# Kernel optimization log

Hardware: AMD Instinct MI355X
Metric: run time of the kernel (lower is better)

The kernel has to match this reference:

```python
import jax, jax.numpy as jnp
import numpy as np

N = 40000      # nodes
E = 640000     # edges
G = 2048       # graphs
D = 128        # emb_dim
T = 10         # num_tasks
L = 5          # layers
ATOM_VOCAB = 64
BOND_VOCAB = 8
BN_EPS = 1e-5


def _bn(x, g, b, m, v):
    # inference-mode BatchNorm1d with running stats
    return (x - m) * jax.lax.rsqrt(v + BN_EPS) * g + b


def setup_inputs() -> dict:
    key = jax.random.key(0)
    ks = jax.random.split(key, 24)
    inp = {
        "x_atom": jax.random.randint(ks[0], (N, 9), 0, ATOM_VOCAB),
        "edge_index": jax.random.randint(ks[1], (2, E), 0, N),
        "edge_attr": jax.random.randint(ks[2], (E, 3), 0, BOND_VOCAB),
        "batch": jnp.sort(jax.random.randint(ks[3], (N,), 0, G)),
        # embedding tables
        "atom_emb": jax.random.normal(ks[4], (9, ATOM_VOCAB, D)) * 0.1,
        "bond_emb": jax.random.normal(ks[5], (L, 3, BOND_VOCAB, D)) * 0.1,
        # per-layer GIN params (stacked over L)
        "eps": jnp.zeros((L,)),
        "W1": jax.random.normal(ks[6], (L, D, 2 * D)) * 0.05,
        "b1": jnp.zeros((L, 2 * D)),
        "g1": jnp.ones((L, 2 * D)),
        "bt1": jnp.zeros((L, 2 * D)),
        "m1": jax.random.normal(ks[7], (L, 2 * D)) * 0.1,
        "v1": jax.random.uniform(ks[8], (L, 2 * D), minval=0.5, maxval=1.5),
        "W2": jax.random.normal(ks[9], (L, 2 * D, D)) * 0.05,
        "b2": jnp.zeros((L, D)),
        # outer BatchNorm per layer
        "gO": jnp.ones((L, D)),
        "btO": jnp.zeros((L, D)),
        "mO": jax.random.normal(ks[10], (L, D)) * 0.1,
        "vO": jax.random.uniform(ks[11], (L, D), minval=0.5, maxval=1.5),
        # prediction head
        "Wp": jax.random.normal(ks[12], (D, T)) * 0.05,
        "bp": jnp.zeros((T,)),
    }
    return inp


def reference(x_atom, edge_index, edge_attr, batch, atom_emb, bond_emb, eps,
              W1, b1, g1, bt1, m1, v1, W2, b2, gO, btO, mO, vO, Wp, bp):
    src, dst = edge_index[0], edge_index[1]
    # AtomEncoder: sum of per-feature embeddings -> [N, D]
    x = atom_emb[jnp.arange(9)[None, :], x_atom].sum(axis=1)
    feat3 = jnp.arange(3)[None, :]
    for i in range(L):
        # BondEncoder for this layer -> [E, D]
        e = bond_emb[i][feat3, edge_attr].sum(axis=1)
        # message: relu(x_j + edge_emb); aggregate: scatter-add at dst
        msg = jax.nn.relu(x[src] + e)
        agg = jax.ops.segment_sum(msg, dst, num_segments=N)
        h = (1.0 + eps[i]) * x + agg
        # MLP: Linear -> BN -> ReLU -> Linear
        h = jax.nn.relu(_bn(h @ W1[i] + b1[i], g1[i], bt1[i], m1[i], v1[i]))
        h = h @ W2[i] + b2[i]
        # outer BN; ReLU after all but last layer (dropout = identity in eval)
        x = _bn(h, gO[i], btO[i], mO[i], vO[i])
        if i < L - 1:
            x = jax.nn.relu(x)
    # global mean pool over graphs
    sums = jax.ops.segment_sum(x, batch, num_segments=G)
    cnt = jax.ops.segment_sum(jnp.ones((N,), x.dtype), batch, num_segments=G)
    pooled = sums / jnp.maximum(cnt, 1.0)[:, None]
    return pooled @ Wp + bp
```

## Files before the change

kernel.cpp:

```cpp
#include <hip/hip_runtime.h>
#include <hip/hip_bf16.h>

#define NN 40000
#define NE 640000
#define NG 2048
#define DD 128
#define NT 10
#define NL 5
#define NB 80

typedef __attribute__((ext_vector_type(8))) short short8;
typedef __attribute__((ext_vector_type(4))) float f32x4;
typedef unsigned short ushort_t;

static __device__ __forceinline__ ushort_t f2b(float f) {
    return __bfloat16_as_ushort(__float2bfloat16(f));
}
static __device__ __forceinline__ float b2f(ushort_t u) {
    return __bfloat162float(__ushort_as_bfloat16(u));
}

__global__ void k_atom(const int* __restrict__ xa, const float* __restrict__ emb,
                       ushort_t* __restrict__ x16) {
    int n = blockIdx.x, d = threadIdx.x;
    __shared__ int idx[9];
    if (d < 9) idx[d] = xa[n * 9 + d];
    __syncthreads();
    float s = 0.f;
#pragma unroll
    for (int f = 0; f < 9; ++f) s += emb[(f * 64 + idx[f]) * DD + d];
    x16[n * DD + d] = f2b(s);
}


__global__ void k_hist(const int* __restrict__ ei, int* __restrict__ deg) {
    int e = blockIdx.x * 256 + threadIdx.x;
    atomicAdd(&deg[ei[NE + e]], 1);
}

__global__ void k_scan1(const int* __restrict__ deg, int* __restrict__ off,
                        int* __restrict__ blksum) {
    int b = blockIdx.x, t = threadIdx.x;
    int i = b * 256 + t;
    __shared__ int s[256];
    int v = (i < NN) ? deg[i] : 0;
    s[t] = v;
    __syncthreads();
    for (int d = 1; d < 256; d <<= 1) {
        int add = (t >= d) ? s[t - d] : 0;
        __syncthreads();
        s[t] += add;
        __syncthreads();
    }
    if (i <= NN) off[i] = s[t] - v;
    if (t == 255) blksum[b] = s[255];
}

__global__ void k_scan2(int* __restrict__ blk) {
    int t = threadIdx.x;
    __shared__ int s[256];
    int v = blk[t];
    s[t] = v;
    __syncthreads();
    for (int d = 1; d < 256; d <<= 1) {
        int add = (t >= d) ? s[t - d] : 0;
        __syncthreads();
        s[t] += add;
        __syncthreads();
    }
    blk[256 + t] = s[t] - v;
}

__global__ void k_scan3(int* __restrict__ off, const int* __restrict__ blk) {
    int b = blockIdx.x, t = threadIdx.x;
    int i = b * 256 + t;
    if (i <= NN) off[i] += blk[256 + b];
}

__global__ void __launch_bounds__(256)
k_bucket(const int* __restrict__ ei, const int* __restrict__ ea,
         const int* __restrict__ off, int* __restrict__ gbk,
         int2* __restrict__ ebuf) {
    __shared__ int hist[NB];
    __shared__ int sbase[NB];
    int t = threadIdx.x;
    int e0 = blockIdx.x * 1024;
    if (t < NB) hist[t] = 0;
    __syncthreads();
    int rank[4], buck[4], rec[4], dstv[4];
#pragma unroll
    for (int k = 0; k < 4; ++k) {
        int e = e0 + k * 256 + t;
        int src = ei[e];
        int dst = ei[NE + e];
        int a0 = ea[e * 3 + 0], a1 = ea[e * 3 + 1], a2 = ea[e * 3 + 2];
        rec[k] = src | ((a0 | (a1 << 3) | (a2 << 6)) << 16);
        dstv[k] = dst;
        int b = dst >> 9;
        buck[k] = b;
        rank[k] = atomicAdd(&hist[b], 1);
    }
    __syncthreads();
    if (t < NB) sbase[t] = atomicAdd(&gbk[t], hist[t]);
    __syncthreads();
#pragma unroll
    for (int k = 0; k < 4; ++k) {
        int b = buck[k];
        int slot = off[b << 9] + sbase[b] + rank[k];
        ebuf[slot] = make_int2(rec[k], dstv[k]);
    }
}

__global__ void k_scatter2(const int2* __restrict__ ebuf, const int* __restrict__ off,
                           int* __restrict__ cursor, int2* __restrict__ epack) {
    int i = blockIdx.x * 256 + threadIdx.x;
    int2 s = ebuf[i];
    int dst = s.y;
    int p = off[dst] + atomicAdd(&cursor[dst], 1);
    epack[p] = make_int2(s.x & 0xFFFF, s.x >> 16);
}

__global__ void k_tables(const float* __restrict__ W1, const float* __restrict__ W2,
                         const float* __restrict__ bemb, ushort_t* __restrict__ W1P,
                         ushort_t* __restrict__ W2P, ushort_t* __restrict__ ebsum16) {
    int tid = blockIdx.x * 256 + threadIdx.x;
    int layer = tid >> 16;
    int r = tid & 65535;
    int half = r >> 15;
    int q = r & 32767;
    int j = q & 7;
    int lane = (q >> 3) & 63;
    if (half == 0) {
        int kk = (q >> 9) & 3;
        int nt = q >> 11;
        int n = nt * 16 + (lane & 15);
        int k = kk * 32 + (lane >> 4) * 8 + j;
        W1P[layer * 32768 + q] = f2b(W1[(layer * DD + k) * 256 + n]);
    } else {
        int kk = (q >> 9) & 7;
        int nt = q >> 12;
        int n = nt * 16 + (lane & 15);
        int k = kk * 32 + (lane >> 4) * 8 + j;
        W2P[layer * 32768 + q] = f2b(W2[(layer * 256 + k) * DD + n]);
    }
    int d = tid & 127;
    int c = (tid >> 7) & 511;
    const float* bl = bemb + (size_t)layer * 3 * 8 * DD;
    ebsum16[tid] = f2b(bl[(c & 7) * DD + d] + bl[(8 + ((c >> 3) & 7)) * DD + d] +
                       bl[(16 + (c >> 6)) * DD + d]);
}

__global__ void __launch_bounds__(256)
k_gather(const ushort_t* __restrict__ xin, const int* __restrict__ off,
         const int2* __restrict__ epack, const ushort_t* __restrict__ ebsum16,
         const float* __restrict__ eps, int layer, ushort_t* __restrict__ h16) {
    int t = threadIdx.x;
    int lane = t & 63;
    int n = blockIdx.x * 4 + (t >> 6);
    const ushort2* x2 = (const ushort2*)xin;
    const ushort2* eb2 = (const ushort2*)ebsum16;
    ushort2 xv = x2[n * 64 + lane];
    float es = 1.f + eps[layer];
    float ax = es * b2f(xv.x), ay = es * b2f(xv.y);
    int p = off[n], p1 = off[n + 1];

    int2 e0, e1, e2, e3;
    bool have = (p + 4 <= p1);
    if (have) { e0 = epack[p]; e1 = epack[p + 1]; e2 = epack[p + 2]; e3 = epack[p + 3]; }
    while (have) {
        int np = p + 4;
        bool nh = (np + 4 <= p1);
        int2 f0, f1, f2, f3;
        if (nh) { f0 = epack[np]; f1 = epack[np + 1]; f2 = epack[np + 2]; f3 = epack[np + 3]; }
        ushort2 v0 = eb2[e0.y * 64 + lane];
        ushort2 s0 = x2[e0.x * 64 + lane];
        ushort2 v1 = eb2[e1.y * 64 + lane];
        ushort2 s1 = x2[e1.x * 64 + lane];
        ushort2 v2 = eb2[e2.y * 64 + lane];
        ushort2 s2 = x2[e2.x * 64 + lane];
        ushort2 v3 = eb2[e3.y * 64 + lane];
        ushort2 s3 = x2[e3.x * 64 + lane];
        ax += fmaxf(b2f(v0.x) + b2f(s0.x), 0.f) + fmaxf(b2f(v1.x) + b2f(s1.x), 0.f) +
              fmaxf(b2f(v2.x) + b2f(s2.x), 0.f) + fmaxf(b2f(v3.x) + b2f(s3.x), 0.f);
        ay += fmaxf(b2f(v0.y) + b2f(s0.y), 0.f) + fmaxf(b2f(v1.y) + b2f(s1.y), 0.f) +
              fmaxf(b2f(v2.y) + b2f(s2.y), 0.f) + fmaxf(b2f(v3.y) + b2f(s3.y), 0.f);
        p = np;
        e0 = f0; e1 = f1; e2 = f2; e3 = f3;
        have = nh;
    }
    for (; p < p1; ++p) {
        int2 er = epack[p];
        ushort2 ev = eb2[er.y * 64 + lane];
        ushort2 sv = x2[er.x * 64 + lane];
        ax += fmaxf(b2f(ev.x) + b2f(sv.x), 0.f);
        ay += fmaxf(b2f(ev.y) + b2f(sv.y), 0.f);
    }
    ushort2 o;
    o.x = f2b(ax);
    o.y = f2b(ay);
    ((ushort2*)h16)[n * 64 + lane] = o;
}

__global__ void __launch_bounds__(256)
k_mlp_mfma(const ushort_t* __restrict__ h16, const ushort_t* __restrict__ W1P,
           const ushort_t* __restrict__ W2P, const float* __restrict__ b1,
           const float* __restrict__ g1, const float* __restrict__ bt1,
           const float* __restrict__ m1, const float* __restrict__ v1,
           const float* __restrict__ b2_, const float* __restrict__ gO,
           const float* __restrict__ btO, const float* __restrict__ mO,
           const float* __restrict__ vO, int relu, ushort_t* __restrict__ xout) {
    __shared__ ushort_t aS[32 * 136];
    __shared__ ushort_t mid[32 * 264];
    int t = threadIdx.x;
    int wave = t >> 6, lane = t & 63;
    int row0 = blockIdx.x * 32;
    int lrow = lane & 15, quad = lane >> 4;

#pragma unroll
    for (int ps = 0; ps < 2; ++ps) {
        int idx = ps * 256 + t;
        int r = idx >> 4, c = (idx & 15) * 8;
        *(short8*)&aS[r * 136 + c] = *(const short8*)&h16[(row0 + r) * DD + c];
    }
    __syncthreads();

    f32x4 acc1[2][4];
#pragma unroll
    for (int rt = 0; rt < 2; ++rt)
#pragma unroll
        for (int i = 0; i < 4; ++i) acc1[rt][i] = (f32x4){0.f, 0.f, 0.f, 0.f};
#pragma unroll
    for (int kk = 0; kk < 4; ++kk) {
        short8 af0 = *(const short8*)&aS[lrow * 136 + kk * 32 + quad * 8];
        short8 af1 = *(const short8*)&aS[(16 + lrow) * 136 + kk * 32 + quad * 8];
#pragma unroll
        for (int i = 0; i < 4; ++i) {
            int nt = wave * 4 + i;
            short8 bf = *(const short8*)&W1P[((nt * 4 + kk) * 64 + lane) * 8];
            acc1[0][i] = __builtin_amdgcn_mfma_f32_16x16x32_bf16(af0, bf, acc1[0][i], 0, 0, 0);
            acc1[1][i] = __builtin_amdgcn_mfma_f32_16x16x32_bf16(af1, bf, acc1[1][i], 0, 0, 0);
        }
    }
#pragma unroll
    for (int i = 0; i < 4; ++i) {
        int col = (wave * 4 + i) * 16 + lrow;
        float s1 = g1[col] * rsqrtf(v1[col] + 1e-5f);
        float sh = bt1[col] - (m1[col] - b1[col]) * s1;
#pragma unroll
        for (int rt = 0; rt < 2; ++rt)
#pragma unroll
            for (int r = 0; r < 4; ++r) {
                int row = rt * 16 + quad * 4 + r;
                float o = acc1[rt][i][r] * s1 + sh;
                mid[row * 264 + col] = f2b(fmaxf(o, 0.f));
            }
    }
    __syncthreads();

    f32x4 acc2[2][2];
#pragma unroll
    for (int rt = 0; rt < 2; ++rt)
#pragma unroll
        for (int i = 0; i < 2; ++i) acc2[rt][i] = (f32x4){0.f, 0.f, 0.f, 0.f};
#pragma unroll
    for (int kk = 0; kk < 8; ++kk) {
        short8 af0 = *(const short8*)&mid[lrow * 264 + kk * 32 + quad * 8];
        short8 af1 = *(const short8*)&mid[(16 + lrow) * 264 + kk * 32 + quad * 8];
#pragma unroll
        for (int i = 0; i < 2; ++i) {
            int nt = wave * 2 + i;
            short8 bf = *(const short8*)&W2P[((nt * 8 + kk) * 64 + lane) * 8];
            acc2[0][i] = __builtin_amdgcn_mfma_f32_16x16x32_bf16(af0, bf, acc2[0][i], 0, 0, 0);
            acc2[1][i] = __builtin_amdgcn_mfma_f32_16x16x32_bf16(af1, bf, acc2[1][i], 0, 0, 0);
        }
    }
#pragma unroll
    for (int i = 0; i < 2; ++i) {
        int col = (wave * 2 + i) * 16 + lrow;
        float s = gO[col] * rsqrtf(vO[col] + 1e-5f);
        float sh = btO[col] - (mO[col] - b2_[col]) * s;
#pragma unroll
        for (int rt = 0; rt < 2; ++rt)
#pragma unroll
            for (int r = 0; r < 4; ++r) {
                int row = rt * 16 + quad * 4 + r;
                float o = acc2[rt][i][r] * s + sh;
                if (relu) o = fmaxf(o, 0.f);
                xout[(row0 + row) * DD + col] = f2b(o);
            }
    }
}

__global__ void k_pool(const ushort_t* __restrict__ x16, const int* __restrict__ batch,
                       float* __restrict__ pooled) {
    int g = blockIdx.x, d = threadIdx.x;
    int lo = 0, hi = NN;
    while (lo < hi) { int m = (lo + hi) >> 1; if (batch[m] < g) lo = m + 1; else hi = m; }
    int start = lo;
    hi = NN;
    while (lo < hi) { int m = (lo + hi) >> 1; if (batch[m] < g + 1) lo = m + 1; else hi = m; }
    int end = lo;
    float s = 0.f;
    for (int n = start; n < end; ++n) s += b2f(x16[n * DD + d]);
    float c = fmaxf((float)(end - start), 1.f);
    pooled[g * DD + d] = s / c;
}

__global__ void k_head(const float* __restrict__ pooled, const float* __restrict__ Wp,
                       const float* __restrict__ bp, float* __restrict__ out) {
    int g = blockIdx.x;
    int d = threadIdx.x;
    __shared__ float p[DD];
    p[d] = pooled[g * DD + d];
    __syncthreads();
    if (d < NT) {
        float acc = bp[d];
#pragma unroll 8
        for (int k = 0; k < DD; ++k) acc = fmaf(p[k], Wp[k * NT + d], acc);
        out[g * NT + d] = acc;
    }
}

extern "C" void kernel_launch(void* const* d_in, const int* in_sizes, int n_in,
                              void* d_out, int out_size, void* d_ws, size_t ws_size,
                              hipStream_t stream) {
    const int* x_atom = (const int*)d_in[0];
    const int* edge_index = (const int*)d_in[1];
    const int* edge_attr = (const int*)d_in[2];
    const int* batch = (const int*)d_in[3];
    const float* atom_emb = (const float*)d_in[4];
    const float* bond_emb = (const float*)d_in[5];
    const float* eps = (const float*)d_in[6];
    const float* W1 = (const float*)d_in[7];
    const float* b1 = (const float*)d_in[8];
    const float* g1 = (const float*)d_in[9];
    const float* bt1 = (const float*)d_in[10];
    const float* m1 = (const float*)d_in[11];
    const float* v1 = (const float*)d_in[12];
    const float* W2 = (const float*)d_in[13];
    const float* b2 = (const float*)d_in[14];
    const float* gO = (const float*)d_in[15];
    const float* btO = (const float*)d_in[16];
    const float* mO = (const float*)d_in[17];
    const float* vO = (const float*)d_in[18];
    const float* Wp = (const float*)d_in[19];
    const float* bp = (const float*)d_in[20];

    ushort_t* x16a = (ushort_t*)d_ws;
    ushort_t* x16b = x16a + NN * DD;
    ushort_t* h16 = x16b + NN * DD;
    float* pooled = (float*)(h16 + NN * DD);
    ushort_t* W1P = (ushort_t*)(pooled + NG * DD);
    ushort_t* W2P = W1P + NL * 32768;
    ushort_t* ebsum16 = W2P + NL * 32768;
    int* deg = (int*)(ebsum16 + NL * 65536);
    int* off = deg + NN;
    int* blk = off + 40064;
    int* cursor = blk + 512;
    int* gbk = cursor + NN;
    int2* epack = (int2*)(gbk + 128);
    int2* ebuf = epack + NE;

    hipMemsetAsync(deg, 0, (NN + 40064 + 512 + NN + 128) * sizeof(int), stream);

    k_tables<<<NL * 65536 / 256, 256, 0, stream>>>(W1, W2, bond_emb, W1P, W2P, ebsum16);
    k_atom<<<NN, DD, 0, stream>>>(x_atom, atom_emb, x16a);

    k_hist<<<NE / 256, 256, 0, stream>>>(edge_index, deg);
    k_scan1<<<157, 256, 0, stream>>>(deg, off, blk);
    k_scan2<<<1, 256, 0, stream>>>(blk);
    k_scan3<<<157, 256, 0, stream>>>(off, blk);
    k_bucket<<<NE / 1024, 256, 0, stream>>>(edge_index, edge_attr, off, gbk, ebuf);
    k_scatter2<<<NE / 256, 256, 0, stream>>>(ebuf, off, cursor, epack);

    for (int i = 0; i < NL; ++i) {
        ushort_t* xin = (i & 1) ? x16b : x16a;
        ushort_t* xout = (i & 1) ? x16a : x16b;
        k_gather<<<NN / 4, 256, 0, stream>>>(xin, off, epack, ebsum16 + i * 65536,
                                             eps, i, h16);
        k_mlp_mfma<<<NN / 32, 256, 0, stream>>>(
            h16, W1P + (size_t)i * 32768, W2P + (size_t)i * 32768, b1 + i * 256,
            g1 + i * 256, bt1 + i * 256, m1 + i * 256, v1 + i * 256, b2 + i * DD,
            gO + i * DD, btO + i * DD, mO + i * DD, vO + i * DD,
            (i < NL - 1) ? 1 : 0, xout);
    }
    k_pool<<<NG, DD, 0, stream>>>(x16b, batch, pooled);
    k_head<<<NG, DD, 0, stream>>>(pooled, Wp, bp, (float*)d_out);
}
```

Before: 435.7 us.

## Fuse setup kernels, merge pool+head, and deepen gather edge prefetch to 8

Merges the table-prep, atom-embedding and degree-histogram kernels into one launch with block-range dispatch, and fuses mean pooling with the prediction head so the pooled buffer is no longer written and reread. The gather loop now prefetches edge records 8 at a time with clamped indices and a predicated tail, replacing the 4-wide loop plus scalar remainder. This raises memory-level parallelism in the main gather and cuts launch overhead. The cost is redundant loads for short adjacency lists and more register pressure in the gather.

```diff
diff --git a/kernel.cpp b/kernel.cpp
--- a/kernel.cpp
+++ b/kernel.cpp
@@ -20,23 +20,56 @@
     return __bfloat162float(__ushort_as_bfloat16(u));
 }
 
-__global__ void k_atom(const int* __restrict__ xa, const float* __restrict__ emb,
-                       ushort_t* __restrict__ x16) {
-    int n = blockIdx.x, d = threadIdx.x;
-    __shared__ int idx[9];
-    if (d < 9) idx[d] = xa[n * 9 + d];
-    __syncthreads();
-    float s = 0.f;
-#pragma unroll
-    for (int f = 0; f < 9; ++f) s += emb[(f * 64 + idx[f]) * DD + d];
-    x16[n * DD + d] = f2b(s);
-}
-
-
-__global__ void k_hist(const int* __restrict__ ei, int* __restrict__ deg) {
-    int e = blockIdx.x * 256 + threadIdx.x;
-    atomicAdd(&deg[ei[NE + e]], 1);
-}
+__global__ void __launch_bounds__(256)
+k_setup(const float* __restrict__ W1, const float* __restrict__ W2,
+        const float* __restrict__ bemb, const int* __restrict__ xa,
+        const float* __restrict__ aemb, const int* __restrict__ ei,
+        ushort_t* __restrict__ W1P, ushort_t* __restrict__ W2P,
+        ushort_t* __restrict__ ebsum16, ushort_t* __restrict__ x16,
+        int* __restrict__ deg) {
+    int b = blockIdx.x, t = threadIdx.x;
+    if (b < 1280) {
+        int tid = b * 256 + t;
+        int layer = tid >> 16;
+        int r = tid & 65535;
+        int half = r >> 15;
+        int q = r & 32767;
+        int j = q & 7;
+        int lane = (q >> 3) & 63;
+        if (half == 0) {
+            int kk = (q >> 9) & 3;
+            int nt = q >> 11;
+            int n = nt * 16 + (lane & 15);
+            int k = kk * 32 + (lane >> 4) * 8 + j;
+            W1P[layer * 32768 + q] = f2b(W1[(layer * DD + k) * 256 + n]);
+        } else {
+            int kk = (q >> 9) & 7;
+            int nt = q >> 12;
+            int n = nt * 16 + (lane & 15);
+            int k = kk * 32 + (lane >> 4) * 8 + j;
+            W2P[layer * 32768 + q] = f2b(W2[(layer * 256 + k) * DD + n]);
+        }
+        int d = tid & 127;
+        int c = (tid >> 7) & 511;
+        const float* bl = bemb + (size_t)layer * 3 * 8 * DD;
+        ebsum16[tid] = f2b(bl[(c & 7) * DD + d] + bl[(8 + ((c >> 3) & 7)) * DD + d] +
+                           bl[(16 + (c >> 6)) * DD + d]);
+    } else if (b < 21280) {
+        int half = t >> 7, d = t & 127;
+        int n = (b - 1280) * 2 + half;
+        __shared__ int idx[2][9];
+        if (d < 9) idx[half][d] = xa[n * 9 + d];
+        __syncthreads();
+        float s = 0.f;
+#pragma unroll
+        for (int f = 0; f < 9; ++f) s += aemb[(f * 64 + idx[half][f]) * DD + d];
+        x16[n * DD + d] = f2b(s);
+    } else {
+        int e = (b - 21280) * 256 + t;
+        atomicAdd(&deg[ei[NE + e]], 1);
+    }
+}
+
 
 __global__ void k_scan1(const int* __restrict__ deg, int* __restrict__ off,
                         int* __restrict__ blksum) {
@@ -118,36 +151,6 @@
     int dst = s.y;
     int p = off[dst] + atomicAdd(&cursor[dst], 1);
     epack[p] = make_int2(s.x & 0xFFFF, s.x >> 16);
-}
-
-__global__ void k_tables(const float* __restrict__ W1, const float* __restrict__ W2,
-                         const float* __restrict__ bemb, ushort_t* __restrict__ W1P,
-                         ushort_t* __restrict__ W2P, ushort_t* __restrict__ ebsum16) {
-    int tid = blockIdx.x * 256 + threadIdx.x;
-    int layer = tid >> 16;
-    int r = tid & 65535;
-    int half = r >> 15;
-    int q = r & 32767;
-    int j = q & 7;
-    int lane = (q >> 3) & 63;
-    if (half == 0) {
-        int kk = (q >> 9) & 3;
-        int nt = q >> 11;
-        int n = nt * 16 + (lane & 15);
-        int k = kk * 32 + (lane >> 4) * 8 + j;
-        W1P[layer * 32768 + q] = f2b(W1[(layer * DD + k) * 256 + n]);
-    } else {
-        int kk = (q >> 9) & 7;
-        int nt = q >> 12;
-        int n = nt * 16 + (lane & 15);
-        int k = kk * 32 + (lane >> 4) * 8 + j;
-        W2P[layer * 32768 + q] = f2b(W2[(layer * 256 + k) * DD + n]);
-    }
-    int d = tid & 127;
-    int c = (tid >> 7) & 511;
-    const float* bl = bemb + (size_t)layer * 3 * 8 * DD;
-    ebsum16[tid] = f2b(bl[(c & 7) * DD + d] + bl[(8 + ((c >> 3) & 7)) * DD + d] +
-                       bl[(16 + (c >> 6)) * DD + d]);
 }
 
 __global__ void __launch_bounds__(256)
@@ -164,36 +167,35 @@
     float ax = es * b2f(xv.x), ay = es * b2f(xv.y);
     int p = off[n], p1 = off[n + 1];
 
-    int2 e0, e1, e2, e3;
-    bool have = (p + 4 <= p1);
-    if (have) { e0 = epack[p]; e1 = epack[p + 1]; e2 = epack[p + 2]; e3 = epack[p + 3]; }
-    while (have) {
-        int np = p + 4;
-        bool nh = (np + 4 <= p1);
-        int2 f0, f1, f2, f3;
-        if (nh) { f0 = epack[np]; f1 = epack[np + 1]; f2 = epack[np + 2]; f3 = epack[np + 3]; }
-        ushort2 v0 = eb2[e0.y * 64 + lane];
-        ushort2 s0 = x2[e0.x * 64 + lane];
-        ushort2 v1 = eb2[e1.y * 64 + lane];
-        ushort2 s1 = x2[e1.x * 64 + lane];
-        ushort2 v2 = eb2[e2.y * 64 + lane];
-        ushort2 s2 = x2[e2.x * 64 + lane];
-        ushort2 v3 = eb2[e3.y * 64 + lane];
-        ushort2 s3 = x2[e3.x * 64 + lane];
-        ax += fmaxf(b2f(v0.x) + b2f(s0.x), 0.f) + fmaxf(b2f(v1.x) + b2f(s1.x), 0.f) +
-              fmaxf(b2f(v2.x) + b2f(s2.x), 0.f) + fmaxf(b2f(v3.x) + b2f(s3.x), 0.f);
-        ay += fmaxf(b2f(v0.y) + b2f(s0.y), 0.f) + fmaxf(b2f(v1.y) + b2f(s1.y), 0.f) +
-              fmaxf(b2f(v2.y) + b2f(s2.y), 0.f) + fmaxf(b2f(v3.y) + b2f(s3.y), 0.f);
-        p = np;
-        e0 = f0; e1 = f1; e2 = f2; e3 = f3;
-        have = nh;
-    }
-    for (; p < p1; ++p) {
-        int2 er = epack[p];
-        ushort2 ev = eb2[er.y * 64 + lane];
-        ushort2 sv = x2[er.x * 64 + lane];
-        ax += fmaxf(b2f(ev.x) + b2f(sv.x), 0.f);
-        ay += fmaxf(b2f(ev.y) + b2f(sv.y), 0.f);
+    if (p < p1) {
+        int2 e[8];
+#pragma unroll
+        for (int j = 0; j < 8; ++j) e[j] = epack[(p + j < p1) ? p + j : p1 - 1];
+        while (p < p1) {
+            int np = p + 8;
+            int2 f[8];
+            bool nh = np < p1;
+            if (nh) {
+#pragma unroll
+                for (int j = 0; j < 8; ++j) f[j] = epack[(np + j < p1) ? np + j : p1 - 1];
+            }
+            ushort2 v[8], s[8];
+#pragma unroll
+            for (int j = 0; j < 8; ++j) {
+                v[j] = eb2[e[j].y * 64 + lane];
+                s[j] = x2[e[j].x * 64 + lane];
+            }
+#pragma unroll
+            for (int j = 0; j < 8; ++j) {
+                if (p + j < p1) {
+                    ax += fmaxf(b2f(v[j].x) + b2f(s[j].x), 0.f);
+                    ay += fmaxf(b2f(v[j].y) + b2f(s[j].y), 0.f);
+                }
+            }
+#pragma unroll
+            for (int j = 0; j < 8; ++j) e[j] = f[j];
+            p = np;
+        }
     }
     ushort2 o;
     o.x = f2b(ax);
@@ -291,8 +293,10 @@
     }
 }
 
-__global__ void k_pool(const ushort_t* __restrict__ x16, const int* __restrict__ batch,
-                       float* __restrict__ pooled) {
+__global__ void k_poolhead(const ushort_t* __restrict__ x16,
+                           const int* __restrict__ batch,
+                           const float* __restrict__ Wp, const float* __restrict__ bp,
+                           float* __restrict__ out) {
     int g = blockIdx.x, d = threadIdx.x;
     int lo = 0, hi = NN;
     while (lo < hi) { int m = (lo + hi) >> 1; if (batch[m] < g) lo = m + 1; else hi = m; }
@@ -303,15 +307,8 @@
     float s = 0.f;
     for (int n = start; n < end; ++n) s += b2f(x16[n * DD + d]);
     float c = fmaxf((float)(end - start), 1.f);
-    pooled[g * DD + d] = s / c;
-}
-
-__global__ void k_head(const float* __restrict__ pooled, const float* __restrict__ Wp,
-                       const float* __restrict__ bp, float* __restrict__ out) {
-    int g = blockIdx.x;
-    int d = threadIdx.x;
     __shared__ float p[DD];
-    p[d] = pooled[g * DD + d];
+    p[d] = s / c;
     __syncthreads();
     if (d < NT) {
         float acc = bp[d];
@@ -349,8 +346,7 @@
     ushort_t* x16a = (ushort_t*)d_ws;
     ushort_t* x16b = x16a + NN * DD;
     ushort_t* h16 = x16b + NN * DD;
-    float* pooled = (float*)(h16 + NN * DD);
-    ushort_t* W1P = (ushort_t*)(pooled + NG * DD);
+    ushort_t* W1P = h16 + NN * DD;
     ushort_t* W2P = W1P + NL * 32768;
     ushort_t* ebsum16 = W2P + NL * 32768;
     int* deg = (int*)(ebsum16 + NL * 65536);
@@ -363,10 +359,8 @@
 
     hipMemsetAsync(deg, 0, (NN + 40064 + 512 + NN + 128) * sizeof(int), stream);
 
-    k_tables<<<NL * 65536 / 256, 256, 0, stream>>>(W1, W2, bond_emb, W1P, W2P, ebsum16);
-    k_atom<<<NN, DD, 0, stream>>>(x_atom, atom_emb, x16a);
-
-    k_hist<<<NE / 256, 256, 0, stream>>>(edge_index, deg);
+    k_setup<<<23780, 256, 0, stream>>>(W1, W2, bond_emb, x_atom, atom_emb,
+                                       edge_index, W1P, W2P, ebsum16, x16a, deg);
     k_scan1<<<157, 256, 0, stream>>>(deg, off, blk);
     k_scan2<<<1, 256, 0, stream>>>(blk);
     k_scan3<<<157, 256, 0, stream>>>(off, blk);
@@ -384,6 +378,5 @@
             gO + i * DD, btO + i * DD, mO + i * DD, vO + i * DD,
             (i < NL - 1) ? 1 : 0, xout);
     }
-    k_pool<<<NG, DD, 0, stream>>>(x16b, batch, pooled);
-    k_head<<<NG, DD, 0, stream>>>(pooled, Wp, bp, (float*)d_out);
-}
+    k_poolhead<<<NG, DD, 0, stream>>>(x16b, batch, Wp, bp, (float*)d_out);
+}
```

Result: slower. 470.1 us (+7.9%).
